# Kernel tuning notes

Measured on AMD Instinct MI355X. Metric: run time of the kernel, lower is better.

Reference implementation:

```python
import jax, jax.numpy as jnp
import numpy as np

NUM_GRAPHS = 100  # batch of graphs for pooling (dgl.max_nodes / WeightAndSum)


def _glorot(k, shape):
    lim = np.sqrt(6.0 / (shape[0] + shape[1])).astype(np.float32)
    return jax.random.uniform(k, shape, jnp.float32, -lim, lim)


def setup_inputs() -> dict:
    key = jax.random.key(0)
    ks = jax.random.split(key, 10)
    N, E, D, H = 100000, 1600000, 128, 128
    node_feats = jax.random.normal(ks[0], (N, D), dtype=jnp.float32)
    src = jax.random.randint(ks[1], (E,), 0, N, dtype=jnp.int32)
    dst = jax.random.randint(ks[2], (E,), 0, N, dtype=jnp.int32)
    graph_ids = jnp.sort(jax.random.randint(ks[3], (N,), 0, NUM_GRAPHS, dtype=jnp.int32))
    W1 = _glorot(ks[4], (D, H)); b1 = jnp.zeros((H,), jnp.float32)
    W2 = _glorot(ks[5], (H, H)); b2 = jnp.zeros((H,), jnp.float32)
    W3 = _glorot(ks[6], (H, H)); b3 = jnp.zeros((H,), jnp.float32)
    W_pool = _glorot(ks[7], (H, 1)); b_pool = jnp.zeros((1,), jnp.float32)
    return {"node_feats": node_feats, "src": src, "dst": dst, "graph_ids": graph_ids,
            "W1": W1, "b1": b1, "W2": W2, "b2": b2, "W3": W3, "b3": b3,
            "W_pool": W_pool, "b_pool": b_pool}


def _gcn_layer(h, W, b, src, dst, norm_src, norm_dst, N):
    # DGL GraphConv, norm='both': D_dst^{-1/2} (A^T (D_src^{-1/2} X W)) + b
    h = (h * norm_src[:, None]) @ W                      # [N, H]
    agg = jax.ops.segment_sum(h[src], dst, num_segments=N)  # gather + scatter-add
    return agg * norm_dst[:, None] + b


def reference(node_feats, src, dst, graph_ids, W1, b1, W2, b2, W3, b3, W_pool, b_pool):
    N = node_feats.shape[0]
    # dgl.add_self_loop (allow_zero_in_degree=False)
    loops = jnp.arange(N, dtype=src.dtype)
    src_sl = jnp.concatenate([src, loops])
    dst_sl = jnp.concatenate([dst, loops])
    ones = jnp.ones(src_sl.shape, jnp.float32)
    out_deg = jax.ops.segment_sum(ones, src_sl, num_segments=N)
    in_deg = jax.ops.segment_sum(ones, dst_sl, num_segments=N)
    norm_src = jax.lax.rsqrt(jnp.maximum(out_deg, 1.0))
    norm_dst = jax.lax.rsqrt(jnp.maximum(in_deg, 1.0))
    h = node_feats
    for W, b in ((W1, b1), (W2, b2), (W3, b3)):
        h = jax.nn.relu(_gcn_layer(h, W, b, src_sl, dst_sl, norm_src, norm_dst, N))
    # pooling_func: WeightAndSum (sigmoid-gated weighted sum per graph) + max_nodes
    w = jax.nn.sigmoid(h @ W_pool + b_pool)              # [N, 1]
    g_sum = jax.ops.segment_sum(h * w, graph_ids, num_segments=NUM_GRAPHS)
    g_max = jax.ops.segment_max(h, graph_ids, num_segments=NUM_GRAPHS)
    return jnp.concatenate([g_sum, g_max], axis=1)       # [G, 2H]
```

## Files before the change

### kernel.cpp

```cpp
#include <hip/hip_runtime.h>
#include <hip/hip_bf16.h>

#define DIM 128
#define CAP 64
#define NBMAX 64
#define BCAP 36864

typedef __attribute__((ext_vector_type(8))) short bf16x8;
typedef __attribute__((ext_vector_type(4))) float f32x4;
union U16 { uint4 u; bf16x8 b; };

__device__ __forceinline__ unsigned short f2bf(float f) {
    unsigned u = __float_as_uint(f);
    unsigned r = (u + 0x7fffu + ((u >> 16) & 1u)) >> 16;
    return (unsigned short)r;
}
__device__ __forceinline__ unsigned pack2bf(float a, float b) {
    return (unsigned)f2bf(a) | ((unsigned)f2bf(b) << 16);
}
__device__ __forceinline__ float2 unpack2bf(unsigned v) {
    float2 r;
    r.x = __uint_as_float(v << 16);
    r.y = __uint_as_float(v & 0xffff0000u);
    return r;
}
__device__ __forceinline__ void accum8s(float* acc, uint4 v, float s) {
    float2 f0 = unpack2bf(v.x), f1 = unpack2bf(v.y);
    float2 f2 = unpack2bf(v.z), f3 = unpack2bf(v.w);
    acc[0] += s * f0.x; acc[1] += s * f0.y; acc[2] += s * f1.x; acc[3] += s * f1.y;
    acc[4] += s * f2.x; acc[5] += s * f2.y; acc[6] += s * f3.x; acc[7] += s * f3.y;
}

__global__ __launch_bounds__(256) void k_bin(const int* __restrict__ src,
                                             const int* __restrict__ dst, int E,
                                             unsigned* __restrict__ binD,
                                             unsigned short* __restrict__ binS,
                                             int* __restrict__ cntD,
                                             int* __restrict__ cntS, int NB, int binGrid,
                                             const float* __restrict__ W1,
                                             const float* __restrict__ W2,
                                             const float* __restrict__ W3,
                                             unsigned* __restrict__ wT1g,
                                             unsigned* __restrict__ wT2g,
                                             unsigned* __restrict__ wT3g) {
    __shared__ int hD[NBMAX], hS[NBMAX], bD[NBMAX], bS[NBMAX];
    int t = threadIdx.x;
    if ((int)blockIdx.x >= binGrid) {
        int w = blockIdx.x - binGrid;
        const float* Wsrc = (w == 0) ? W1 : (w == 1) ? W2 : W3;
        unsigned* wTg = (w == 0) ? wT1g : (w == 1) ? wT2g : wT3g;
        int n = t >> 1;
        int kp0 = (t & 1) * 32;
#pragma unroll
        for (int i = 0; i < 32; i++) {
            int kp = kp0 + i;
            wTg[n * 64 + kp] = pack2bf(Wsrc[(2 * kp) * DIM + n], Wsrc[(2 * kp + 1) * DIM + n]);
        }
        return;
    }
    if (t < NB) { hD[t] = 0; hS[t] = 0; }
    __syncthreads();
    int e0 = blockIdx.x * 1024 + t * 4;
    int s[4], d[4];
    bool v[4];
#pragma unroll
    for (int i = 0; i < 4; i++) {
        v[i] = (e0 + i) < E;
        s[i] = 0; d[i] = 0;
        if (v[i]) { s[i] = src[e0 + i]; d[i] = dst[e0 + i]; }
    }
#pragma unroll
    for (int i = 0; i < 4; i++) {
        if (v[i]) {
            atomicAdd(&hD[d[i] >> 11], 1);
            atomicAdd(&hS[s[i] >> 11], 1);
        }
    }
    __syncthreads();
    if (t < NB) {
        bD[t] = atomicAdd(&cntD[t], hD[t]);
        bS[t] = atomicAdd(&cntS[t], hS[t]);
        hD[t] = 0; hS[t] = 0;
    }
    __syncthreads();
#pragma unroll
    for (int i = 0; i < 4; i++) {
        if (v[i]) {
            int bd = d[i] >> 11;
            int r = atomicAdd(&hD[bd], 1);
            int idx = bD[bd] + r;
            if (idx < BCAP)
                binD[bd * BCAP + idx] = ((unsigned)(d[i] & 2047) << 17) | (unsigned)s[i];
            int bs = s[i] >> 11;
            int r2 = atomicAdd(&hS[bs], 1);
            int idx2 = bS[bs] + r2;
            if (idx2 < BCAP) binS[bs * BCAP + idx2] = (unsigned short)(s[i] & 2047);
        }
    }
}

__global__ __launch_bounds__(256) void k_mega(const unsigned* __restrict__ binD,
                                              const unsigned short* __restrict__ binS,
                                              const int* __restrict__ cntD,
                                              const int* __restrict__ cntS,
                                              int* __restrict__ in_cnt,
                                              int* __restrict__ out_cnt,
                                              int* __restrict__ csr_pad,
                                              const float* __restrict__ x,
                                              const unsigned* __restrict__ wT1g,
                                              unsigned* __restrict__ xwb, int N,
                                              int NB) {
    __shared__ __align__(16) char smem[34816];
    int bid = blockIdx.x;
    int t = threadIdx.x;

    if (bid < NB) {
        int* cnt = (int*)smem;
        for (int j = t; j < 2048; j += 256) cnt[j] = 0;
        __syncthreads();
        int base = bid << 11;
        int nE = cntD[bid];
        if (nE > BCAP) nE = BCAP;
        const unsigned* bb = &binD[bid * BCAP];
        for (int i = t; i < nE; i += 256) {
            unsigned e = bb[i];
            int dl = (int)(e >> 17);
            int sv = (int)(e & 0x1FFFFu);
            int pos = atomicAdd(&cnt[dl], 1);
            if (pos < CAP) csr_pad[(size_t)(base + dl) * CAP + pos] = sv;
        }
        __syncthreads();
        for (int j = t; j < 2048; j += 256) {
            int n = base + j;
            if (n < N) in_cnt[n] = cnt[j];
        }
        return;
    }
    if (bid < 2 * NB) {
        int b = bid - NB;
        int* hist = (int*)smem;
        for (int j = t; j < 2048; j += 256) hist[j] = 0;
        __syncthreads();
        int base = b << 11;
        int nE = cntS[b];
        if (nE > BCAP) nE = BCAP;
        const unsigned short* bs = &binS[b * BCAP];
        for (int i = t; i < nE; i += 256) {
            atomicAdd(&hist[(int)bs[i]], 1);
        }
        __syncthreads();
        for (int j = t; j < 2048; j += 256) {
            int n = base + j;
            if (n < N) out_cnt[n] = hist[j];
        }
        return;
    }
    int gb = bid - 2 * NB;
    unsigned* wT = (unsigned*)smem;
#pragma unroll
    for (int i = 0; i < 8; i++) {
        int idx = t + i * 256;
        int row = idx >> 4;
        int col = idx & 15;
        *(uint4*)&wT[row * 68 + col * 4] = ((const uint4*)wT1g)[idx];
    }
    __syncthreads();
    int wave = t >> 6, lane = t & 63;
    int quad = lane >> 4, c = lane & 15;
    int m = gb * 64 + wave * 16 + c;
    bool mv = m < N;
    f32x4 acc[8];
#pragma unroll
    for (int i = 0; i < 8; i++) acc[i] = (f32x4){0.f, 0.f, 0.f, 0.f};

#pragma unroll
    for (int ks = 0; ks < 4; ks++) {
        U16 av;
        if (mv) {
            const float4* xr = (const float4*)&x[(size_t)m * DIM + ks * 32 + quad * 8];
            float4 f0 = xr[0], f1 = xr[1];
            av.u.x = pack2bf(f0.x, f0.y);
            av.u.y = pack2bf(f0.z, f0.w);
            av.u.z = pack2bf(f1.x, f1.y);
            av.u.w = pack2bf(f1.z, f1.w);
        } else {
            av.u = make_uint4(0, 0, 0, 0);
        }
#pragma unroll
        for (int cb = 0; cb < 8; cb++) {
            U16 bv;
            bv.u = *(const uint4*)&wT[(cb * 16 + c) * 68 + ks * 16 + quad * 4];
            acc[cb] = __builtin_amdgcn_mfma_f32_16x16x32_bf16(av.b, bv.b, acc[cb], 0, 0, 0);
        }
    }
    int rowBase = gb * 64 + wave * 16 + quad * 4;
#pragma unroll
    for (int r = 0; r < 4; r++) {
        int rowN = rowBase + r;
#pragma unroll
        for (int cb = 0; cb < 8; cb++) {
            float v = acc[cb][r];
            float vn = __shfl_xor(v, 1, 64);
            if (((c & 1) == 0) && rowN < N)
                xwb[rowN * 64 + cb * 8 + (c >> 1)] = pack2bf(v, vn);
        }
    }
}

__global__ __launch_bounds__(256) void k_agg1(const uint4* __restrict__ xwb4,
                                              const int* __restrict__ in_cnt,
                                              const int* __restrict__ out_cnt,
                                              const int* __restrict__ csr_pad,
                                              const float* __restrict__ bias,
                                              uint4* __restrict__ hb4, int N) {
    int gid = blockIdx.x * blockDim.x + threadIdx.x;
    int n = gid >> 6;
    int lane = gid & 63;
    if (n >= N) return;
    int quad = lane >> 4;
    int c = lane & 15;

    float acc[8];
#pragma unroll
    for (int i = 0; i < 8; i++) acc[i] = 0.f;

    if (quad == 0) {
        float sn = rsqrtf((float)(out_cnt[n] + 1));
        accum8s(acc, xwb4[n * 16 + c], sn);
    }
    int deg_true = in_cnt[n];
    int deg = deg_true > CAP ? CAP : deg_true;
    const int* row = &csr_pad[(size_t)n * CAP];
    int p = 0;
    for (; p + 16 <= deg; p += 16) {
        int s0 = row[p + quad];
        int s1 = row[p + 4 + quad];
        int s2 = row[p + 8 + quad];
        int s3 = row[p + 12 + quad];
        uint4 v0 = xwb4[s0 * 16 + c];
        uint4 v1 = xwb4[s1 * 16 + c];
        uint4 v2 = xwb4[s2 * 16 + c];
        uint4 v3 = xwb4[s3 * 16 + c];
        float n0 = rsqrtf((float)(out_cnt[s0] + 1));
        float n1 = rsqrtf((float)(out_cnt[s1] + 1));
        float n2 = rsqrtf((float)(out_cnt[s2] + 1));
        float n3 = rsqrtf((float)(out_cnt[s3] + 1));
        accum8s(acc, v0, n0);
        accum8s(acc, v1, n1);
        accum8s(acc, v2, n2);
        accum8s(acc, v3, n3);
    }
    for (; p + 8 <= deg; p += 8) {
        int s0 = row[p + quad];
        int s1 = row[p + 4 + quad];
        uint4 v0 = xwb4[s0 * 16 + c];
        uint4 v1 = xwb4[s1 * 16 + c];
        float n0 = rsqrtf((float)(out_cnt[s0] + 1));
        float n1 = rsqrtf((float)(out_cnt[s1] + 1));
        accum8s(acc, v0, n0);
        accum8s(acc, v1, n1);
    }
    for (; p < deg; p += 4) {
        int pe = p + quad;
        int s = row[pe < deg ? pe : p];
        uint4 v = xwb4[s * 16 + c];
        float ns = rsqrtf((float)(out_cnt[s] + 1));
        if (pe < deg) accum8s(acc, v, ns);
    }
#pragma unroll
    for (int i = 0; i < 8; i++) {
        acc[i] += __shfl_xor(acc[i], 16, 64);
        acc[i] += __shfl_xor(acc[i], 32, 64);
    }
    float ndv = rsqrtf((float)(deg_true + 1));
    if (quad == 0) {
        float4 b0 = ((const float4*)bias)[2 * c];
        float4 b1 = ((const float4*)bias)[2 * c + 1];
        uint4 w;
        w.x = pack2bf(fmaxf(acc[0] * ndv + b0.x, 0.f), fmaxf(acc[1] * ndv + b0.y, 0.f));
        w.y = pack2bf(fmaxf(acc[2] * ndv + b0.z, 0.f), fmaxf(acc[3] * ndv + b0.w, 0.f));
        w.z = pack2bf(fmaxf(acc[4] * ndv + b1.x, 0.f), fmaxf(acc[5] * ndv + b1.y, 0.f));
        w.w = pack2bf(fmaxf(acc[6] * ndv + b1.z, 0.f), fmaxf(acc[7] * ndv + b1.w, 0.f));
        hb4[n * 16 + c] = w;
    }
}

__global__ __launch_bounds__(256) void k_xw_mfma(const unsigned* __restrict__ hb,
                                                 const int* __restrict__ out_cnt,
                                                 const unsigned* __restrict__ wTg,
                                                 unsigned* __restrict__ xwb, int N) {
    __shared__ unsigned wT[128 * 68];
    int t = threadIdx.x;
#pragma unroll
    for (int i = 0; i < 8; i++) {
        int idx = t + i * 256;
        int row = idx >> 4;
        int col = idx & 15;
        *(uint4*)&wT[row * 68 + col * 4] = ((const uint4*)wTg)[idx];
    }
    __syncthreads();
    int wave = t >> 6, lane = t & 63;
    int quad = lane >> 4, c = lane & 15;
    int m = blockIdx.x * 64 + wave * 16 + c;
    bool mv = m < N;
    f32x4 acc[8];
#pragma unroll
    for (int i = 0; i < 8; i++) acc[i] = (f32x4){0.f, 0.f, 0.f, 0.f};

#pragma unroll
    for (int ks = 0; ks < 4; ks++) {
        U16 av;
        if (mv) av.u = *(const uint4*)&hb[m * 64 + ks * 16 + quad * 4];
        else av.u = make_uint4(0, 0, 0, 0);
#pragma unroll
        for (int cb = 0; cb < 8; cb++) {
            U16 bv;
            bv.u = *(const uint4*)&wT[(cb * 16 + c) * 68 + ks * 16 + quad * 4];
            acc[cb] = __builtin_amdgcn_mfma_f32_16x16x32_bf16(av.b, bv.b, acc[cb], 0, 0, 0);
        }
    }
    int rowBase = blockIdx.x * 64 + wave * 16 + quad * 4;
#pragma unroll
    for (int r = 0; r < 4; r++) {
        int rowN = rowBase + r;
        float nrm = (rowN < N) ? rsqrtf((float)(out_cnt[rowN] + 1)) : 0.f;
#pragma unroll
        for (int cb = 0; cb < 8; cb++) {
            float v = acc[cb][r] * nrm;
            float vn = __shfl_xor(v, 1, 64);
            if (((c & 1) == 0) && rowN < N)
                xwb[rowN * 64 + cb * 8 + (c >> 1)] = pack2bf(v, vn);
        }
    }
}

template <bool GATED>
__device__ __forceinline__ void agg_body(const uint4* __restrict__ xwb4,
                                         const int* __restrict__ in_cnt,
                                         const int* __restrict__ csr_pad,
                                         const float* __restrict__ bias,
                                         uint4* __restrict__ hb4,
                                         const float* __restrict__ Wp,
                                         const float* __restrict__ bp,
                                         float* __restrict__ wg, int N) {
    int gid = blockIdx.x * blockDim.x + threadIdx.x;
    int n = gid >> 6;
    int lane = gid & 63;
    if (n >= N) return;
    int quad = lane >> 4;
    int c = lane & 15;

    float acc[8];
#pragma unroll
    for (int i = 0; i < 8; i++) acc[i] = 0.f;

    if (quad == 0) {
        accum8s(acc, xwb4[n * 16 + c], 1.f);
    }
    int deg_true = in_cnt[n];
    int deg = deg_true > CAP ? CAP : deg_true;
    const int* row = &csr_pad[(size_t)n * CAP];
    int p = 0;
    for (; p + 16 <= deg; p += 16) {
        int s0 = row[p + quad];
        int s1 = row[p + 4 + quad];
        int s2 = row[p + 8 + quad];
        int s3 = row[p + 12 + quad];
        uint4 v0 = xwb4[s0 * 16 + c];
        uint4 v1 = xwb4[s1 * 16 + c];
        uint4 v2 = xwb4[s2 * 16 + c];
        uint4 v3 = xwb4[s3 * 16 + c];
        accum8s(acc, v0, 1.f);
        accum8s(acc, v1, 1.f);
        accum8s(acc, v2, 1.f);
        accum8s(acc, v3, 1.f);
    }
    for (; p + 8 <= deg; p += 8) {
        int s0 = row[p + quad];
        int s1 = row[p + 4 + quad];
        uint4 v0 = xwb4[s0 * 16 + c];
        uint4 v1 = xwb4[s1 * 16 + c];
        accum8s(acc, v0, 1.f);
        accum8s(acc, v1, 1.f);
    }
    for (; p < deg; p += 4) {
        int pe = p + quad;
        int s = row[pe < deg ? pe : p];
        uint4 v = xwb4[s * 16 + c];
        if (pe < deg) accum8s(acc, v, 1.f);
    }
#pragma unroll
    for (int i = 0; i < 8; i++) {
        acc[i] += __shfl_xor(acc[i], 16, 64);
        acc[i] += __shfl_xor(acc[i], 32, 64);
    }
    float ndv = rsqrtf((float)(deg_true + 1));
    float4 b0 = ((const float4*)bias)[2 * c];
    float4 b1 = ((const float4*)bias)[2 * c + 1];
    float o[8];
    o[0] = fmaxf(acc[0] * ndv + b0.x, 0.f);
    o[1] = fmaxf(acc[1] * ndv + b0.y, 0.f);
    o[2] = fmaxf(acc[2] * ndv + b0.z, 0.f);
    o[3] = fmaxf(acc[3] * ndv + b0.w, 0.f);
    o[4] = fmaxf(acc[4] * ndv + b1.x, 0.f);
    o[5] = fmaxf(acc[5] * ndv + b1.y, 0.f);
    o[6] = fmaxf(acc[6] * ndv + b1.z, 0.f);
    o[7] = fmaxf(acc[7] * ndv + b1.w, 0.f);
    if (quad == 0) {
        uint4 w;
        w.x = pack2bf(o[0], o[1]);
        w.y = pack2bf(o[2], o[3]);
        w.z = pack2bf(o[4], o[5]);
        w.w = pack2bf(o[6], o[7]);
        hb4[n * 16 + c] = w;
    }
    if (GATED) {
        float s = 0.f;
        if (quad == 0) {
            float4 w0 = ((const float4*)Wp)[2 * c];
            float4 w1 = ((const float4*)Wp)[2 * c + 1];
            s = o[0] * w0.x + o[1] * w0.y + o[2] * w0.z + o[3] * w0.w +
                o[4] * w1.x + o[5] * w1.y + o[6] * w1.z + o[7] * w1.w;
        }
        s += __shfl_xor(s, 1, 64);
        s += __shfl_xor(s, 2, 64);
        s += __shfl_xor(s, 4, 64);
        s += __shfl_xor(s, 8, 64);
        if (lane == 0) wg[n] = 1.f / (1.f + expf(-(s + bp[0])));
    }
}

__global__ __launch_bounds__(256) void k_agg(const uint4* __restrict__ xwb4,
                                             const int* __restrict__ in_cnt,
                                             const int* __restrict__ csr_pad,
                                             const float* __restrict__ bias,
                                             uint4* __restrict__ hb4, int N) {
    agg_body<false>(xwb4, in_cnt, csr_pad, bias, hb4, nullptr, nullptr, nullptr, N);
}

__global__ __launch_bounds__(256) void k_agg_gate(const uint4* __restrict__ xwb4,
                                                  const int* __restrict__ in_cnt,
                                                  const int* __restrict__ csr_pad,
                                                  const float* __restrict__ bias,
                                                  uint4* __restrict__ hb4,
                                                  const float* __restrict__ Wp,
                                                  const float* __restrict__ bp,
                                                  float* __restrict__ wg, int N) {
    agg_body<true>(xwb4, in_cnt, csr_pad, bias, hb4, Wp, bp, wg, N);
}

__device__ __forceinline__ int lower_bound(const int* a, int n, int key) {
    int lo = 0, hi = n;
    while (lo < hi) {
        int m = (lo + hi) >> 1;
        if (a[m] < key) lo = m + 1;
        else hi = m;
    }
    return lo;
}

__global__ __launch_bounds__(64) void k_pool(const unsigned* __restrict__ hb,
                                             const float* __restrict__ wg,
                                             const int* __restrict__ gids,
                                             float* __restrict__ out, int N) {
    int g = blockIdx.x >> 4;
    int part = blockIdx.x & 15;
    int t = threadIdx.x;
    int start = lower_bound(gids, N, g);
    int end = lower_bound(gids, N, g + 1);
    float2 sum = {0.f, 0.f}, mx = {0.f, 0.f};
    for (int n = start + part; n < end; n += 16) {
        float w = wg[n];
        float2 v = unpack2bf(hb[n * 64 + t]);
        sum.x += v.x * w;
        sum.y += v.y * w;
        mx.x = fmaxf(mx.x, v.x);
        mx.y = fmaxf(mx.y, v.y);
    }
    atomicAdd(&out[g * 256 + 2 * t], sum.x);
    atomicAdd(&out[g * 256 + 2 * t + 1], sum.y);
    atomicMax((int*)&out[g * 256 + 128 + 2 * t], __float_as_int(mx.x));
    atomicMax((int*)&out[g * 256 + 128 + 2 * t + 1], __float_as_int(mx.y));
}

extern "C" void kernel_launch(void* const* d_in, const int* in_sizes, int n_in,
                              void* d_out, int out_size, void* d_ws, size_t ws_size,
                              hipStream_t stream) {
    const float* node_feats = (const float*)d_in[0];
    const int* src = (const int*)d_in[1];
    const int* dst = (const int*)d_in[2];
    const int* gids = (const int*)d_in[3];
    const float* W1 = (const float*)d_in[4];
    const float* b1 = (const float*)d_in[5];
    const float* W2 = (const float*)d_in[6];
    const float* b2 = (const float*)d_in[7];
    const float* W3 = (const float*)d_in[8];
    const float* b3 = (const float*)d_in[9];
    const float* Wp = (const float*)d_in[10];
    const float* bp = (const float*)d_in[11];
    float* out = (float*)d_out;

    const int N = in_sizes[3];
    const int E = in_sizes[1];
    const int G = out_size / 256;
    const int NB = (N + 2047) >> 11;

    char* ws = (char*)d_ws;
    size_t o = 0;
    int* cntD = (int*)(ws + o);          o += NBMAX * 4;
    int* cntS = (int*)(ws + o);          o += NBMAX * 4;
    size_t zero_bytes = o;
    int* in_cnt = (int*)(ws + o);        o += (size_t)N * 4;
    int* out_cnt = (int*)(ws + o);       o += (size_t)N * 4;
    float* wg = (float*)(ws + o);        o += (size_t)N * 4;
    o = (o + 15) & ~15ull;
    unsigned* wT1g = (unsigned*)(ws + o); o += 8192 * 4;
    unsigned* wT2g = (unsigned*)(ws + o); o += 8192 * 4;
    unsigned* wT3g = (unsigned*)(ws + o); o += 8192 * 4;
    unsigned* binD = (unsigned*)(ws + o); o += (size_t)NBMAX * BCAP * 4;
    unsigned short* binS = (unsigned short*)(ws + o); o += (size_t)NBMAX * BCAP * 2;
    o = (o + 15) & ~15ull;
    int* csr_pad = (int*)(ws + o);       o += (size_t)N * CAP * 4;
    unsigned* xwb = (unsigned*)(ws + o); o += (size_t)N * 64 * 4;
    unsigned* hb = (unsigned*)(ws + o);  o += (size_t)N * 64 * 4;
    (void)ws_size;

    (void)hipMemsetAsync(d_ws, 0, zero_bytes, stream);
    (void)hipMemsetAsync(d_out, 0, (size_t)out_size * 4, stream);

    int binGrid = (E + 1023) / 1024;
    int mmGrid = (N + 63) / 64;
    int aggGrid = ((N * 64) + 255) / 256;

    k_bin<<<binGrid + 3, 256, 0, stream>>>(src, dst, E, binD, binS, cntD, cntS, NB, binGrid,
                                           W1, W2, W3, wT1g, wT2g, wT3g);
    k_mega<<<2 * NB + mmGrid, 256, 0, stream>>>(binD, binS, cntD, cntS, in_cnt, out_cnt,
                                                csr_pad, node_feats, wT1g, xwb, N, NB);
    k_agg1<<<aggGrid, 256, 0, stream>>>((const uint4*)xwb, in_cnt, out_cnt, csr_pad, b1,
                                        (uint4*)hb, N);
    k_xw_mfma<<<mmGrid, 256, 0, stream>>>(hb, out_cnt, wT2g, xwb, N);
    k_agg<<<aggGrid, 256, 0, stream>>>((const uint4*)xwb, in_cnt, csr_pad, b2,
                                       (uint4*)hb, N);
    k_xw_mfma<<<mmGrid, 256, 0, stream>>>(hb, out_cnt, wT3g, xwb, N);
    k_agg_gate<<<aggGrid, 256, 0, stream>>>((const uint4*)xwb, in_cnt, csr_pad, b3,
                                            (uint4*)hb, Wp, bp, wg, N);
    k_pool<<<G * 16, 64, 0, stream>>>(hb, wg, gids, out, N);
}
```

Measured before the change: 473.4 us.

## Split per-bin CSR build and degree histogram across multiple blocks

Each destination/source bin of edges was processed by a single block in k_mega; now every bin is split across CSPLIT=8 blocks. Each block builds a local histogram, reserves slot offsets with global atomics on in_cnt, then scatters into the padded CSR. Out-degree counts are accumulated the same way with global atomics. This spreads the CSR build over more CUs to remove the serial tail of a few long blocks. In exchange it reads each bin twice, adds global atomics, and zeroes in_cnt/out_cnt with a memset.

New measurement: 454.4 us. -4.0%, faster.

```diff
diff --git a/kernel.cpp b/kernel.cpp
--- a/kernel.cpp
+++ b/kernel.cpp
@@ -5,6 +5,7 @@
 #define CAP 64
 #define NBMAX 64
 #define BCAP 36864
+#define CSPLIT 8
 
 typedef __attribute__((ext_vector_type(8))) short bf16x8;
 typedef __attribute__((ext_vector_type(4))) float f32x4;
@@ -114,48 +115,91 @@
     int bid = blockIdx.x;
     int t = threadIdx.x;
 
-    if (bid < NB) {
-        int* cnt = (int*)smem;
-        for (int j = t; j < 2048; j += 256) cnt[j] = 0;
+    if (bid < NB * CSPLIT) {
+        int b = bid / CSPLIT;
+        int sub = bid - b * CSPLIT;
+        int* h = (int*)smem;
+        int* bArr = ((int*)smem) + 2048;
+        for (int j = t; j < 2048; j += 256) h[j] = 0;
         __syncthreads();
-        int base = bid << 11;
-        int nE = cntD[bid];
+        int base = b << 11;
+        int nE = cntD[b];
         if (nE > BCAP) nE = BCAP;
-        const unsigned* bb = &binD[bid * BCAP];
-        for (int i = t; i < nE; i += 256) {
-            unsigned e = bb[i];
-            int dl = (int)(e >> 17);
-            int sv = (int)(e & 0x1FFFFu);
-            int pos = atomicAdd(&cnt[dl], 1);
-            if (pos < CAP) csr_pad[(size_t)(base + dl) * CAP + pos] = sv;
+        int chunk = (nE + CSPLIT - 1) / CSPLIT;
+        int i0 = sub * chunk;
+        int i1 = i0 + chunk;
+        if (i1 > nE) i1 = nE;
+        const unsigned* bb = &binD[b * BCAP];
+        for (int i = i0 + t * 4; i < i1; i += 1024) {
+            unsigned e[4];
+            int k = i1 - i;
+            if (k > 4) k = 4;
+#pragma unroll
+            for (int j = 0; j < 4; j++)
+                if (j < k) e[j] = bb[i + j];
+#pragma unroll
+            for (int j = 0; j < 4; j++)
+                if (j < k) atomicAdd(&h[e[j] >> 17], 1);
         }
         __syncthreads();
         for (int j = t; j < 2048; j += 256) {
-            int n = base + j;
-            if (n < N) in_cnt[n] = cnt[j];
+            int hv = h[j];
+            bArr[j] = hv ? atomicAdd(&in_cnt[base + j], hv) : 0;
+            h[j] = 0;
+        }
+        __syncthreads();
+        for (int i = i0 + t * 4; i < i1; i += 1024) {
+            unsigned e[4];
+            int k = i1 - i;
+            if (k > 4) k = 4;
+#pragma unroll
+            for (int j = 0; j < 4; j++)
+                if (j < k) e[j] = bb[i + j];
+#pragma unroll
+            for (int j = 0; j < 4; j++)
+                if (j < k) {
+                    int dl = (int)(e[j] >> 17);
+                    int pos = bArr[dl] + atomicAdd(&h[dl], 1);
+                    if (pos < CAP)
+                        csr_pad[(size_t)(base + dl) * CAP + pos] = (int)(e[j] & 0x1FFFFu);
+                }
         }
         return;
     }
-    if (bid < 2 * NB) {
-        int b = bid - NB;
+    if (bid < 2 * NB * CSPLIT) {
+        int bb2 = bid - NB * CSPLIT;
+        int b = bb2 / CSPLIT;
+        int sub = bb2 - b * CSPLIT;
         int* hist = (int*)smem;
         for (int j = t; j < 2048; j += 256) hist[j] = 0;
         __syncthreads();
         int base = b << 11;
         int nE = cntS[b];
         if (nE > BCAP) nE = BCAP;
+        int chunk = (nE + CSPLIT - 1) / CSPLIT;
+        int i0 = sub * chunk;
+        int i1 = i0 + chunk;
+        if (i1 > nE) i1 = nE;
         const unsigned short* bs = &binS[b * BCAP];
-        for (int i = t; i < nE; i += 256) {
-            atomicAdd(&hist[(int)bs[i]], 1);
+        for (int i = i0 + t * 4; i < i1; i += 1024) {
+            unsigned short e[4];
+            int k = i1 - i;
+            if (k > 4) k = 4;
+#pragma unroll
+            for (int j = 0; j < 4; j++)
+                if (j < k) e[j] = bs[i + j];
+#pragma unroll
+            for (int j = 0; j < 4; j++)
+                if (j < k) atomicAdd(&hist[(int)e[j]], 1);
         }
         __syncthreads();
         for (int j = t; j < 2048; j += 256) {
-            int n = base + j;
-            if (n < N) out_cnt[n] = hist[j];
+            int hv = hist[j];
+            if (hv) atomicAdd(&out_cnt[base + j], hv);
         }
         return;
     }
-    int gb = bid - 2 * NB;
+    int gb = bid - 2 * NB * CSPLIT;
     unsigned* wT = (unsigned*)smem;
 #pragma unroll
     for (int i = 0; i < 8; i++) {
@@ -509,9 +553,9 @@
     size_t o = 0;
     int* cntD = (int*)(ws + o);          o += NBMAX * 4;
     int* cntS = (int*)(ws + o);          o += NBMAX * 4;
-    size_t zero_bytes = o;
     int* in_cnt = (int*)(ws + o);        o += (size_t)N * 4;
     int* out_cnt = (int*)(ws + o);       o += (size_t)N * 4;
+    size_t zero_bytes = o;
     float* wg = (float*)(ws + o);        o += (size_t)N * 4;
     o = (o + 15) & ~15ull;
     unsigned* wT1g = (unsigned*)(ws + o); o += 8192 * 4;
@@ -534,8 +578,9 @@
 
     k_bin<<<binGrid + 3, 256, 0, stream>>>(src, dst, E, binD, binS, cntD, cntS, NB, binGrid,
                                            W1, W2, W3, wT1g, wT2g, wT3g);
-    k_mega<<<2 * NB + mmGrid, 256, 0, stream>>>(binD, binS, cntD, cntS, in_cnt, out_cnt,
-                                                csr_pad, node_feats, wT1g, xwb, N, NB);
+    k_mega<<<2 * NB * CSPLIT + mmGrid, 256, 0, stream>>>(binD, binS, cntD, cntS, in_cnt,
+                                                         out_cnt, csr_pad, node_feats,
+                                                         wT1g, xwb, N, NB);
     k_agg1<<<aggGrid, 256, 0, stream>>>((const uint4*)xwb, in_cnt, out_cnt, csr_pad, b1,
                                         (uint4*)hb, N);
     k_xw_mfma<<<mmGrid, 256, 0, stream>>>(hb, out_cnt, wT2g, xwb, N);
```
